# Optimization experiments

Hardware: AMD Instinct MI355X
Metric: run time of the kernel (lower is better)

The kernel has to match this reference:

```python
import jax, jax.numpy as jnp
import numpy as np

N, E, D, K = 60000, 1200000, 64, 3

def setup_inputs() -> dict:
    key = jax.random.key(0)
    k1, k2, k3 = jax.random.split(key, 3)
    feat = jax.random.normal(k1, (N, D), dtype=jnp.float32)
    src = jax.random.randint(k2, (E,), 0, N)
    dst = jax.random.randint(k3, (E,), 0, N)
    lambda_max = jnp.ones((1,), dtype=jnp.float32)
    return {"feat": feat, "src": src, "dst": dst, "lambda_max": lambda_max}

def reference(feat, src, dst, lambda_max):
    n = feat.shape[0]
    # in-degree of each node = number of edges whose dst is that node
    deg = jax.ops.segment_sum(jnp.ones(src.shape[0], dtype=feat.dtype), dst, num_segments=n)
    d_invsqrt = jnp.maximum(deg, 1.0) ** -0.5  # [N]
    d_invsqrt = d_invsqrt[:, None]             # [N,1]
    re_norm = 2.0 / lambda_max                 # [1], broadcasts over nodes/feats

    def unn_laplacian(x):
        # x * D^-1/2 A D^-1/2 via gather over src, scatter-sum to dst
        return d_invsqrt * jax.ops.segment_sum((x * d_invsqrt)[src], dst, num_segments=n)

    X0 = feat
    outs = [X0]
    if K > 1:
        h = unn_laplacian(X0)
        X1 = -re_norm * h + X0 * (re_norm - 1.0)
        outs.append(X1)
    for _ in range(2, K):
        h = unn_laplacian(X1)
        Xi = -2.0 * re_norm * h + X1 * 2.0 * (re_norm - 1.0) - X0
        outs.append(Xi)
        X1, X0 = Xi, X1
    Xt = jnp.concatenate(outs, axis=1)  # [N, K*D]
    return jax.nn.relu(Xt)
```

## Files before the change

kernel.cpp:

```cpp
#include <hip/hip_runtime.h>


#define DF 64
#define BCAP 5760
#define EPT 32

__device__ __forceinline__ unsigned bf16rne(float f) {
    unsigned u = __float_as_uint(f);
    return (u + 0x7FFFu + ((u >> 16) & 1u)) >> 16;
}
__device__ __forceinline__ float bflo(unsigned u) { return __uint_as_float(u << 16); }
__device__ __forceinline__ float bfhi(unsigned u) { return __uint_as_float(u & 0xFFFF0000u); }

__global__ __launch_bounds__(256) void partition_kernel(
    const int* __restrict__ src, const int* __restrict__ dst,
    int* __restrict__ bcursor, int* __restrict__ staged, int E) {
    __shared__ int hist[256];
    __shared__ int base[256];
    int tid = threadIdx.x;
    hist[tid] = 0;
    __syncthreads();
    int e0 = blockIdx.x * (256 * EPT);
    int val[EPT]; int rb[EPT]; int rr[EPT];
    #pragma unroll
    for (int k = 0; k < EPT / 4; k++) {
        int e = e0 + (k * 256 + tid) * 4;
        if (e + 3 < E) {
            int4 s4 = *(const int4*)(src + e);
            int4 d4 = *(const int4*)(dst + e);
            int ss[4] = {s4.x, s4.y, s4.z, s4.w};
            int dd[4] = {d4.x, d4.y, d4.z, d4.w};
            #pragma unroll
            for (int j = 0; j < 4; j++) {
                int b = dd[j] >> 8;
                val[k * 4 + j] = (ss[j] << 8) | (dd[j] & 255);
                rb[k * 4 + j] = b;
                rr[k * 4 + j] = atomicAdd(&hist[b], 1);
            }
        } else {
            #pragma unroll
            for (int j = 0; j < 4; j++) {
                int e1 = e + j;
                if (e1 < E) {
                    int s = src[e1], d = dst[e1];
                    int b = d >> 8;
                    val[k * 4 + j] = (s << 8) | (d & 255);
                    rb[k * 4 + j] = b;
                    rr[k * 4 + j] = atomicAdd(&hist[b], 1);
                } else rb[k * 4 + j] = -1;
            }
        }
    }
    __syncthreads();
    int h = hist[tid];
    base[tid] = h ? atomicAdd(&bcursor[tid], h) : 0;
    __syncthreads();
    #pragma unroll
    for (int k = 0; k < EPT; k++) {
        if (rb[k] >= 0) {
            int pos = base[rb[k]] + rr[k];
            if (pos < BCAP) staged[rb[k] * BCAP + pos] = val[k];
        }
    }
}

__global__ __launch_bounds__(256) void bucket_csr_kernel(
    const int* __restrict__ staged, const int* __restrict__ bcursor,
    int* __restrict__ col, int2* __restrict__ begend,
    float* __restrict__ dinv, int n) {
    __shared__ int sin[BCAP];
    __shared__ __align__(16) int sout[BCAP];
    __shared__ int hist[256];
    __shared__ int scn[256];
    __shared__ int cur[256];
    int tid = threadIdx.x;
    int b = blockIdx.x;
    int cnt = bcursor[b]; if (cnt > BCAP) cnt = BCAP;
    hist[tid] = 0;
    __syncthreads();
    const int* sb = staged + b * BCAP;
    for (int i = tid; i < cnt; i += 256) {
        int e = sb[i];
        sin[i] = e;
        atomicAdd(&hist[e & 255], 1);
    }
    __syncthreads();
    int v = hist[tid];
    scn[tid] = v;
    __syncthreads();
    for (int off = 1; off < 256; off <<= 1) {
        int x = scn[tid];
        int y = (tid >= off) ? scn[tid - off] : 0;
        __syncthreads();
        scn[tid] = x + y;
        __syncthreads();
    }
    int excl = scn[tid] - v;
    cur[tid] = excl;
    __syncthreads();
    for (int i = tid; i < cnt; i += 256) {
        int e = sin[i];
        int pos = atomicAdd(&cur[e & 255], 1);
        sout[pos] = e >> 8;
    }
    __syncthreads();
    int* cb = col + b * BCAP;
    int cnt4 = cnt >> 2;
    for (int i = tid; i < cnt4; i += 256)
        *(int4*)(cb + i * 4) = *(const int4*)(sout + i * 4);
    for (int i = (cnt4 << 2) + tid; i < cnt; i += 256) cb[i] = sout[i];
    int node = (b << 8) + tid;
    if (node < n) {
        int d = hist[tid];
        begend[node] = make_int2(b * BCAP + excl, b * BCAP + excl + d);
        if (d < 1) d = 1;
        dinv[node] = rsqrtf((float)d);
    }
}

__global__ __launch_bounds__(256) void convert_kernel(
    const float* __restrict__ feat, uint2* __restrict__ featb, int total8) {
    int i = blockIdx.x * 256 + threadIdx.x;
    if (i >= total8) return;
    float4 a = *(const float4*)(feat + (size_t)i * 8);
    float4 b = *(const float4*)(feat + (size_t)i * 8 + 4);
    uint2 o;
    (void)o;
    uint4 p;
    p.x = bf16rne(a.x) | (bf16rne(a.y) << 16);
    p.y = bf16rne(a.z) | (bf16rne(a.w) << 16);
    p.z = bf16rne(b.x) | (bf16rne(b.y) << 16);
    p.w = bf16rne(b.z) | (bf16rne(b.w) << 16);
    *(uint4*)((unsigned*)featb + (size_t)i * 4) = p;
}

__global__ __launch_bounds__(256) void prop1_kernel(
    const float* __restrict__ feat, const uint2* __restrict__ featb,
    const int2* __restrict__ begend, const int* __restrict__ col,
    const float* __restrict__ dinv, const float* __restrict__ lambda_max,
    uint2* __restrict__ x1n, float* __restrict__ out, int n) {
    int node = (int)((blockIdx.x * blockDim.x + threadIdx.x) >> 6);
    if (node >= n) return;
    int lane = threadIdx.x & 63;
    int grp = lane >> 4;
    int sub = lane & 15;
    int2 be = begend[node];
    int beg = be.x, end = be.y;
    float4 x0 = *(const float4*)(feat + (size_t)node * DF + sub * 4);
    float dn = dinv[node];
    float rn = 2.0f / lambda_max[0];
    float ax = 0.f, ay = 0.f, az = 0.f, aw = 0.f;
    int i = beg + grp;
    for (; i + 12 < end; i += 16) {
        int s0 = col[i], s1 = col[i + 4], s2 = col[i + 8], s3 = col[i + 12];
        uint2 v0 = featb[(size_t)s0 * 16 + sub];
        uint2 v1 = featb[(size_t)s1 * 16 + sub];
        uint2 v2 = featb[(size_t)s2 * 16 + sub];
        uint2 v3 = featb[(size_t)s3 * 16 + sub];
        float w0 = dinv[s0], w1 = dinv[s1], w2 = dinv[s2], w3 = dinv[s3];
        ax += bflo(v0.x) * w0 + bflo(v1.x) * w1 + bflo(v2.x) * w2 + bflo(v3.x) * w3;
        ay += bfhi(v0.x) * w0 + bfhi(v1.x) * w1 + bfhi(v2.x) * w2 + bfhi(v3.x) * w3;
        az += bflo(v0.y) * w0 + bflo(v1.y) * w1 + bflo(v2.y) * w2 + bflo(v3.y) * w3;
        aw += bfhi(v0.y) * w0 + bfhi(v1.y) * w1 + bfhi(v2.y) * w2 + bfhi(v3.y) * w3;
    }
    for (; i < end; i += 4) {
        int s0 = col[i];
        uint2 v0 = featb[(size_t)s0 * 16 + sub];
        float w0 = dinv[s0];
        ax += bflo(v0.x) * w0; ay += bfhi(v0.x) * w0;
        az += bflo(v0.y) * w0; aw += bfhi(v0.y) * w0;
    }
    ax += __shfl_xor(ax, 16); ax += __shfl_xor(ax, 32);
    ay += __shfl_xor(ay, 16); ay += __shfl_xor(ay, 32);
    az += __shfl_xor(az, 16); az += __shfl_xor(az, 32);
    aw += __shfl_xor(aw, 16); aw += __shfl_xor(aw, 32);
    if (grp == 0) {
        float c1 = rn - 1.0f;
        float4 x1v;
        x1v.x = c1 * x0.x - rn * dn * ax;
        x1v.y = c1 * x0.y - rn * dn * ay;
        x1v.z = c1 * x0.z - rn * dn * az;
        x1v.w = c1 * x0.w - rn * dn * aw;
        uint2 p;
        p.x = bf16rne(x1v.x) | (bf16rne(x1v.y) << 16);
        p.y = bf16rne(x1v.z) | (bf16rne(x1v.w) << 16);
        x1n[(size_t)node * 16 + sub] = p;
        size_t o = (size_t)node * (3 * DF);
        float4 r0 = make_float4(fmaxf(x0.x, 0.f), fmaxf(x0.y, 0.f), fmaxf(x0.z, 0.f), fmaxf(x0.w, 0.f));
        float4 r1 = make_float4(fmaxf(x1v.x, 0.f), fmaxf(x1v.y, 0.f), fmaxf(x1v.z, 0.f), fmaxf(x1v.w, 0.f));
        *(float4*)(out + o + sub * 4) = r0;
        *(float4*)(out + o + DF + sub * 4) = r1;
    }
}

__global__ __launch_bounds__(256) void prop2_kernel(
    const float* __restrict__ feat, const uint2* __restrict__ x1n,
    const int2* __restrict__ begend, const int* __restrict__ col,
    const float* __restrict__ dinv, const float* __restrict__ lambda_max,
    float* __restrict__ out, int n) {
    int node = (int)((blockIdx.x * blockDim.x + threadIdx.x) >> 6);
    if (node >= n) return;
    int lane = threadIdx.x & 63;
    int grp = lane >> 4;
    int sub = lane & 15;
    int2 be = begend[node];
    int beg = be.x, end = be.y;
    float4 x0 = *(const float4*)(feat + (size_t)node * DF + sub * 4);
    uint2 xo = x1n[(size_t)node * 16 + sub];
    float dn = dinv[node];
    float rn = 2.0f / lambda_max[0];
    float ax = 0.f, ay = 0.f, az = 0.f, aw = 0.f;
    int i = beg + grp;
    for (; i + 12 < end; i += 16) {
        int s0 = col[i], s1 = col[i + 4], s2 = col[i + 8], s3 = col[i + 12];
        uint2 v0 = x1n[(size_t)s0 * 16 + sub];
        uint2 v1 = x1n[(size_t)s1 * 16 + sub];
        uint2 v2 = x1n[(size_t)s2 * 16 + sub];
        uint2 v3 = x1n[(size_t)s3 * 16 + sub];
        float w0 = dinv[s0], w1 = dinv[s1], w2 = dinv[s2], w3 = dinv[s3];
        ax += bflo(v0.x) * w0 + bflo(v1.x) * w1 + bflo(v2.x) * w2 + bflo(v3.x) * w3;
        ay += bfhi(v0.x) * w0 + bfhi(v1.x) * w1 + bfhi(v2.x) * w2 + bfhi(v3.x) * w3;
        az += bflo(v0.y) * w0 + bflo(v1.y) * w1 + bflo(v2.y) * w2 + bflo(v3.y) * w3;
        aw += bfhi(v0.y) * w0 + bfhi(v1.y) * w1 + bfhi(v2.y) * w2 + bfhi(v3.y) * w3;
    }
    for (; i < end; i += 4) {
        int s0 = col[i];
        uint2 v0 = x1n[(size_t)s0 * 16 + sub];
        float w0 = dinv[s0];
        ax += bflo(v0.x) * w0; ay += bfhi(v0.x) * w0;
        az += bflo(v0.y) * w0; aw += bfhi(v0.y) * w0;
    }
    ax += __shfl_xor(ax, 16); ax += __shfl_xor(ax, 32);
    ay += __shfl_xor(ay, 16); ay += __shfl_xor(ay, 32);
    az += __shfl_xor(az, 16); az += __shfl_xor(az, 32);
    aw += __shfl_xor(aw, 16); aw += __shfl_xor(aw, 32);
    if (grp == 0) {
        float c2 = 2.0f * (rn - 1.0f);
        float4 x1v = make_float4(bflo(xo.x), bfhi(xo.x), bflo(xo.y), bfhi(xo.y));
        float4 x2v;
        x2v.x = c2 * x1v.x - 2.0f * rn * dn * ax - x0.x;
        x2v.y = c2 * x1v.y - 2.0f * rn * dn * ay - x0.y;
        x2v.z = c2 * x1v.z - 2.0f * rn * dn * az - x0.z;
        x2v.w = c2 * x1v.w - 2.0f * rn * dn * aw - x0.w;
        size_t o = (size_t)node * (3 * DF);
        float4 r2 = make_float4(fmaxf(x2v.x, 0.f), fmaxf(x2v.y, 0.f), fmaxf(x2v.z, 0.f), fmaxf(x2v.w, 0.f));
        *(float4*)(out + o + 2 * DF + sub * 4) = r2;
    }
}

extern "C" void kernel_launch(void* const* d_in, const int* in_sizes, int n_in,
                              void* d_out, int out_size, void* d_ws, size_t ws_size,
                              hipStream_t stream) {
    const float* feat = (const float*)d_in[0];
    const int* src = (const int*)d_in[1];
    const int* dst = (const int*)d_in[2];
    const float* lambda_max = (const float*)d_in[3];
    const int n = in_sizes[0] / DF;
    const int E = in_sizes[1];
    float* out = (float*)d_out;

    const int nb = (n + 255) >> 8;

    auto align256 = [](size_t x) { return (x + 255) & ~(size_t)255; };
    char* ws = (char*)d_ws;
    int* bcursor = (int*)ws;  ws += align256(256 * sizeof(int));
    float* dinv = (float*)ws; ws += align256((size_t)n * sizeof(float));
    int2* begend = (int2*)ws; ws += align256((size_t)n * sizeof(int2));
    int* col = (int*)ws;      ws += align256((size_t)nb * BCAP * sizeof(int));
    int* staged = (int*)ws;
    uint2* featb = (uint2*)ws; ws += align256((size_t)n * DF * 2);
    uint2* x1n = (uint2*)ws;

    hipMemsetAsync(bcursor, 0, 256 * sizeof(int), stream);
    partition_kernel<<<(E + 256 * EPT - 1) / (256 * EPT), 256, 0, stream>>>(
        src, dst, bcursor, staged, E);
    bucket_csr_kernel<<<nb, 256, 0, stream>>>(staged, bcursor, col, begend, dinv, n);
    convert_kernel<<<(n * DF / 8 + 255) / 256, 256, 0, stream>>>(feat, featb, n * DF / 8);
    prop1_kernel<<<(n + 3) / 4, 256, 0, stream>>>(feat, featb, begend, col, dinv, lambda_max, x1n, out, n);
    prop2_kernel<<<(n + 3) / 4, 256, 0, stream>>>(feat, x1n, begend, col, dinv, lambda_max, out, n);
}
```

Measured before the change: 174.7 us.

## Fuse all graph-build and propagation stages into one cooperative persistent kernel

Replaces the memset and five separate launches (partition, bucket CSR, bf16 convert, two propagation passes) with a single cooperative kernel. The stages are separated by grid-wide syncs, and the grid is sized from occupancy across 256 CUs. Shared memory for the partition and CSR phases is overlaid in a union, and the partition tile is halved (EPT 16). The staged buffer now gets its own workspace region because the conversion runs first. The aim is to remove launch gaps and inter-kernel drain. The cost is lower occupancy: the roughly 48KB shared-memory union applies to the gather phases too, which then run as grid-stride loops with grid.sync overhead.

```diff
diff --git a/kernel.cpp b/kernel.cpp
--- a/kernel.cpp
+++ b/kernel.cpp
@@ -1,9 +1,12 @@
 #include <hip/hip_runtime.h>
+#include <hip/hip_cooperative_groups.h>
+
+namespace cg = cooperative_groups;
 
 
 #define DF 64
 #define BCAP 5760
-#define EPT 32
+#define EPT 16
 
 __device__ __forceinline__ unsigned bf16rne(float f) {
     unsigned u = __float_as_uint(f);
@@ -12,239 +15,235 @@
 __device__ __forceinline__ float bflo(unsigned u) { return __uint_as_float(u << 16); }
 __device__ __forceinline__ float bfhi(unsigned u) { return __uint_as_float(u & 0xFFFF0000u); }
 
-__global__ __launch_bounds__(256) void partition_kernel(
-    const int* __restrict__ src, const int* __restrict__ dst,
-    int* __restrict__ bcursor, int* __restrict__ staged, int E) {
-    __shared__ int hist[256];
-    __shared__ int base[256];
-    int tid = threadIdx.x;
-    hist[tid] = 0;
-    __syncthreads();
-    int e0 = blockIdx.x * (256 * EPT);
-    int val[EPT]; int rb[EPT]; int rr[EPT];
-    #pragma unroll
-    for (int k = 0; k < EPT / 4; k++) {
-        int e = e0 + (k * 256 + tid) * 4;
-        if (e + 3 < E) {
-            int4 s4 = *(const int4*)(src + e);
-            int4 d4 = *(const int4*)(dst + e);
-            int ss[4] = {s4.x, s4.y, s4.z, s4.w};
-            int dd[4] = {d4.x, d4.y, d4.z, d4.w};
-            #pragma unroll
-            for (int j = 0; j < 4; j++) {
-                int b = dd[j] >> 8;
-                val[k * 4 + j] = (ss[j] << 8) | (dd[j] & 255);
-                rb[k * 4 + j] = b;
-                rr[k * 4 + j] = atomicAdd(&hist[b], 1);
+__global__ __launch_bounds__(256) void fused_kernel(
+    const float* __restrict__ feat, const int* __restrict__ src,
+    const int* __restrict__ dst, const float* __restrict__ lambda_max,
+    int* __restrict__ bcursor, int* __restrict__ staged,
+    int* __restrict__ col, int2* __restrict__ begend,
+    float* __restrict__ dinv, uint2* __restrict__ featb,
+    uint2* __restrict__ x1n, float* __restrict__ out,
+    int n, int E, int nb, int nRounds) {
+    __shared__ __align__(16) union {
+        struct { int hist[256]; int base[256]; } part;
+        struct { int sin[BCAP]; int sout[BCAP]; int hist[256]; int scn[256]; int cur[256]; } csr;
+    } sh;
+    cg::grid_group grid = cg::this_grid();
+    const int tid = threadIdx.x;
+    const int gsize = gridDim.x;
+
+    if (blockIdx.x == 0) bcursor[tid] = 0;
+    {
+        int total8 = n * DF / 8;
+        for (int i = blockIdx.x * 256 + tid; i < total8; i += gsize * 256) {
+            float4 a = *(const float4*)(feat + (size_t)i * 8);
+            float4 b = *(const float4*)(feat + (size_t)i * 8 + 4);
+            uint4 p;
+            p.x = bf16rne(a.x) | (bf16rne(a.y) << 16);
+            p.y = bf16rne(a.z) | (bf16rne(a.w) << 16);
+            p.z = bf16rne(b.x) | (bf16rne(b.y) << 16);
+            p.w = bf16rne(b.z) | (bf16rne(b.w) << 16);
+            *(uint4*)((unsigned*)featb + (size_t)i * 4) = p;
+        }
+    }
+    grid.sync();
+
+    for (int r = blockIdx.x; r < nRounds; r += gsize) {
+        sh.part.hist[tid] = 0;
+        __syncthreads();
+        int e0 = r * (256 * EPT);
+        int val[EPT]; int rb[EPT]; int rr[EPT];
+        #pragma unroll
+        for (int k = 0; k < EPT / 4; k++) {
+            int e = e0 + (k * 256 + tid) * 4;
+            if (e + 3 < E) {
+                int4 s4 = *(const int4*)(src + e);
+                int4 d4 = *(const int4*)(dst + e);
+                int ss[4] = {s4.x, s4.y, s4.z, s4.w};
+                int dd[4] = {d4.x, d4.y, d4.z, d4.w};
+                #pragma unroll
+                for (int j = 0; j < 4; j++) {
+                    int b = dd[j] >> 8;
+                    val[k * 4 + j] = (ss[j] << 8) | (dd[j] & 255);
+                    rb[k * 4 + j] = b;
+                    rr[k * 4 + j] = atomicAdd(&sh.part.hist[b], 1);
+                }
+            } else {
+                #pragma unroll
+                for (int j = 0; j < 4; j++) {
+                    int e1 = e + j;
+                    if (e1 < E) {
+                        int s = src[e1], d = dst[e1];
+                        int b = d >> 8;
+                        val[k * 4 + j] = (s << 8) | (d & 255);
+                        rb[k * 4 + j] = b;
+                        rr[k * 4 + j] = atomicAdd(&sh.part.hist[b], 1);
+                    } else rb[k * 4 + j] = -1;
+                }
             }
-        } else {
-            #pragma unroll
-            for (int j = 0; j < 4; j++) {
-                int e1 = e + j;
-                if (e1 < E) {
-                    int s = src[e1], d = dst[e1];
-                    int b = d >> 8;
-                    val[k * 4 + j] = (s << 8) | (d & 255);
-                    rb[k * 4 + j] = b;
-                    rr[k * 4 + j] = atomicAdd(&hist[b], 1);
-                } else rb[k * 4 + j] = -1;
+        }
+        __syncthreads();
+        int h = sh.part.hist[tid];
+        sh.part.base[tid] = h ? atomicAdd(&bcursor[tid], h) : 0;
+        __syncthreads();
+        #pragma unroll
+        for (int k = 0; k < EPT; k++) {
+            if (rb[k] >= 0) {
+                int pos = sh.part.base[rb[k]] + rr[k];
+                if (pos < BCAP) staged[rb[k] * BCAP + pos] = val[k];
             }
         }
-    }
-    __syncthreads();
-    int h = hist[tid];
-    base[tid] = h ? atomicAdd(&bcursor[tid], h) : 0;
-    __syncthreads();
-    #pragma unroll
-    for (int k = 0; k < EPT; k++) {
-        if (rb[k] >= 0) {
-            int pos = base[rb[k]] + rr[k];
-            if (pos < BCAP) staged[rb[k] * BCAP + pos] = val[k];
-        }
-    }
-}
-
-__global__ __launch_bounds__(256) void bucket_csr_kernel(
-    const int* __restrict__ staged, const int* __restrict__ bcursor,
-    int* __restrict__ col, int2* __restrict__ begend,
-    float* __restrict__ dinv, int n) {
-    __shared__ int sin[BCAP];
-    __shared__ __align__(16) int sout[BCAP];
-    __shared__ int hist[256];
-    __shared__ int scn[256];
-    __shared__ int cur[256];
-    int tid = threadIdx.x;
-    int b = blockIdx.x;
-    int cnt = bcursor[b]; if (cnt > BCAP) cnt = BCAP;
-    hist[tid] = 0;
-    __syncthreads();
-    const int* sb = staged + b * BCAP;
-    for (int i = tid; i < cnt; i += 256) {
-        int e = sb[i];
-        sin[i] = e;
-        atomicAdd(&hist[e & 255], 1);
-    }
-    __syncthreads();
-    int v = hist[tid];
-    scn[tid] = v;
-    __syncthreads();
-    for (int off = 1; off < 256; off <<= 1) {
-        int x = scn[tid];
-        int y = (tid >= off) ? scn[tid - off] : 0;
-        __syncthreads();
-        scn[tid] = x + y;
-        __syncthreads();
-    }
-    int excl = scn[tid] - v;
-    cur[tid] = excl;
-    __syncthreads();
-    for (int i = tid; i < cnt; i += 256) {
-        int e = sin[i];
-        int pos = atomicAdd(&cur[e & 255], 1);
-        sout[pos] = e >> 8;
-    }
-    __syncthreads();
-    int* cb = col + b * BCAP;
-    int cnt4 = cnt >> 2;
-    for (int i = tid; i < cnt4; i += 256)
-        *(int4*)(cb + i * 4) = *(const int4*)(sout + i * 4);
-    for (int i = (cnt4 << 2) + tid; i < cnt; i += 256) cb[i] = sout[i];
-    int node = (b << 8) + tid;
-    if (node < n) {
-        int d = hist[tid];
-        begend[node] = make_int2(b * BCAP + excl, b * BCAP + excl + d);
-        if (d < 1) d = 1;
-        dinv[node] = rsqrtf((float)d);
-    }
-}
-
-__global__ __launch_bounds__(256) void convert_kernel(
-    const float* __restrict__ feat, uint2* __restrict__ featb, int total8) {
-    int i = blockIdx.x * 256 + threadIdx.x;
-    if (i >= total8) return;
-    float4 a = *(const float4*)(feat + (size_t)i * 8);
-    float4 b = *(const float4*)(feat + (size_t)i * 8 + 4);
-    uint2 o;
-    (void)o;
-    uint4 p;
-    p.x = bf16rne(a.x) | (bf16rne(a.y) << 16);
-    p.y = bf16rne(a.z) | (bf16rne(a.w) << 16);
-    p.z = bf16rne(b.x) | (bf16rne(b.y) << 16);
-    p.w = bf16rne(b.z) | (bf16rne(b.w) << 16);
-    *(uint4*)((unsigned*)featb + (size_t)i * 4) = p;
-}
-
-__global__ __launch_bounds__(256) void prop1_kernel(
-    const float* __restrict__ feat, const uint2* __restrict__ featb,
-    const int2* __restrict__ begend, const int* __restrict__ col,
-    const float* __restrict__ dinv, const float* __restrict__ lambda_max,
-    uint2* __restrict__ x1n, float* __restrict__ out, int n) {
-    int node = (int)((blockIdx.x * blockDim.x + threadIdx.x) >> 6);
-    if (node >= n) return;
-    int lane = threadIdx.x & 63;
-    int grp = lane >> 4;
-    int sub = lane & 15;
-    int2 be = begend[node];
-    int beg = be.x, end = be.y;
-    float4 x0 = *(const float4*)(feat + (size_t)node * DF + sub * 4);
-    float dn = dinv[node];
-    float rn = 2.0f / lambda_max[0];
-    float ax = 0.f, ay = 0.f, az = 0.f, aw = 0.f;
-    int i = beg + grp;
-    for (; i + 12 < end; i += 16) {
-        int s0 = col[i], s1 = col[i + 4], s2 = col[i + 8], s3 = col[i + 12];
-        uint2 v0 = featb[(size_t)s0 * 16 + sub];
-        uint2 v1 = featb[(size_t)s1 * 16 + sub];
-        uint2 v2 = featb[(size_t)s2 * 16 + sub];
-        uint2 v3 = featb[(size_t)s3 * 16 + sub];
-        float w0 = dinv[s0], w1 = dinv[s1], w2 = dinv[s2], w3 = dinv[s3];
-        ax += bflo(v0.x) * w0 + bflo(v1.x) * w1 + bflo(v2.x) * w2 + bflo(v3.x) * w3;
-        ay += bfhi(v0.x) * w0 + bfhi(v1.x) * w1 + bfhi(v2.x) * w2 + bfhi(v3.x) * w3;
-        az += bflo(v0.y) * w0 + bflo(v1.y) * w1 + bflo(v2.y) * w2 + bflo(v3.y) * w3;
-        aw += bfhi(v0.y) * w0 + bfhi(v1.y) * w1 + bfhi(v2.y) * w2 + bfhi(v3.y) * w3;
-    }
-    for (; i < end; i += 4) {
-        int s0 = col[i];
-        uint2 v0 = featb[(size_t)s0 * 16 + sub];
-        float w0 = dinv[s0];
-        ax += bflo(v0.x) * w0; ay += bfhi(v0.x) * w0;
-        az += bflo(v0.y) * w0; aw += bfhi(v0.y) * w0;
-    }
-    ax += __shfl_xor(ax, 16); ax += __shfl_xor(ax, 32);
-    ay += __shfl_xor(ay, 16); ay += __shfl_xor(ay, 32);
-    az += __shfl_xor(az, 16); az += __shfl_xor(az, 32);
-    aw += __shfl_xor(aw, 16); aw += __shfl_xor(aw, 32);
-    if (grp == 0) {
-        float c1 = rn - 1.0f;
-        float4 x1v;
-        x1v.x = c1 * x0.x - rn * dn * ax;
-        x1v.y = c1 * x0.y - rn * dn * ay;
-        x1v.z = c1 * x0.z - rn * dn * az;
-        x1v.w = c1 * x0.w - rn * dn * aw;
-        uint2 p;
-        p.x = bf16rne(x1v.x) | (bf16rne(x1v.y) << 16);
-        p.y = bf16rne(x1v.z) | (bf16rne(x1v.w) << 16);
-        x1n[(size_t)node * 16 + sub] = p;
-        size_t o = (size_t)node * (3 * DF);
-        float4 r0 = make_float4(fmaxf(x0.x, 0.f), fmaxf(x0.y, 0.f), fmaxf(x0.z, 0.f), fmaxf(x0.w, 0.f));
-        float4 r1 = make_float4(fmaxf(x1v.x, 0.f), fmaxf(x1v.y, 0.f), fmaxf(x1v.z, 0.f), fmaxf(x1v.w, 0.f));
-        *(float4*)(out + o + sub * 4) = r0;
-        *(float4*)(out + o + DF + sub * 4) = r1;
-    }
-}
-
-__global__ __launch_bounds__(256) void prop2_kernel(
-    const float* __restrict__ feat, const uint2* __restrict__ x1n,
-    const int2* __restrict__ begend, const int* __restrict__ col,
-    const float* __restrict__ dinv, const float* __restrict__ lambda_max,
-    float* __restrict__ out, int n) {
-    int node = (int)((blockIdx.x * blockDim.x + threadIdx.x) >> 6);
-    if (node >= n) return;
-    int lane = threadIdx.x & 63;
-    int grp = lane >> 4;
-    int sub = lane & 15;
-    int2 be = begend[node];
-    int beg = be.x, end = be.y;
-    float4 x0 = *(const float4*)(feat + (size_t)node * DF + sub * 4);
-    uint2 xo = x1n[(size_t)node * 16 + sub];
-    float dn = dinv[node];
-    float rn = 2.0f / lambda_max[0];
-    float ax = 0.f, ay = 0.f, az = 0.f, aw = 0.f;
-    int i = beg + grp;
-    for (; i + 12 < end; i += 16) {
-        int s0 = col[i], s1 = col[i + 4], s2 = col[i + 8], s3 = col[i + 12];
-        uint2 v0 = x1n[(size_t)s0 * 16 + sub];
-        uint2 v1 = x1n[(size_t)s1 * 16 + sub];
-        uint2 v2 = x1n[(size_t)s2 * 16 + sub];
-        uint2 v3 = x1n[(size_t)s3 * 16 + sub];
-        float w0 = dinv[s0], w1 = dinv[s1], w2 = dinv[s2], w3 = dinv[s3];
-        ax += bflo(v0.x) * w0 + bflo(v1.x) * w1 + bflo(v2.x) * w2 + bflo(v3.x) * w3;
-        ay += bfhi(v0.x) * w0 + bfhi(v1.x) * w1 + bfhi(v2.x) * w2 + bfhi(v3.x) * w3;
-        az += bflo(v0.y) * w0 + bflo(v1.y) * w1 + bflo(v2.y) * w2 + bflo(v3.y) * w3;
-        aw += bfhi(v0.y) * w0 + bfhi(v1.y) * w1 + bfhi(v2.y) * w2 + bfhi(v3.y) * w3;
-    }
-    for (; i < end; i += 4) {
-        int s0 = col[i];
-        uint2 v0 = x1n[(size_t)s0 * 16 + sub];
-        float w0 = dinv[s0];
-        ax += bflo(v0.x) * w0; ay += bfhi(v0.x) * w0;
-        az += bflo(v0.y) * w0; aw += bfhi(v0.y) * w0;
-    }
-    ax += __shfl_xor(ax, 16); ax += __shfl_xor(ax, 32);
-    ay += __shfl_xor(ay, 16); ay += __shfl_xor(ay, 32);
-    az += __shfl_xor(az, 16); az += __shfl_xor(az, 32);
-    aw += __shfl_xor(aw, 16); aw += __shfl_xor(aw, 32);
-    if (grp == 0) {
-        float c2 = 2.0f * (rn - 1.0f);
-        float4 x1v = make_float4(bflo(xo.x), bfhi(xo.x), bflo(xo.y), bfhi(xo.y));
-        float4 x2v;
-        x2v.x = c2 * x1v.x - 2.0f * rn * dn * ax - x0.x;
-        x2v.y = c2 * x1v.y - 2.0f * rn * dn * ay - x0.y;
-        x2v.z = c2 * x1v.z - 2.0f * rn * dn * az - x0.z;
-        x2v.w = c2 * x1v.w - 2.0f * rn * dn * aw - x0.w;
-        size_t o = (size_t)node * (3 * DF);
-        float4 r2 = make_float4(fmaxf(x2v.x, 0.f), fmaxf(x2v.y, 0.f), fmaxf(x2v.z, 0.f), fmaxf(x2v.w, 0.f));
-        *(float4*)(out + o + 2 * DF + sub * 4) = r2;
+        __syncthreads();
+    }
+    grid.sync();
+
+    for (int b = blockIdx.x; b < nb; b += gsize) {
+        int cnt = bcursor[b]; if (cnt > BCAP) cnt = BCAP;
+        sh.csr.hist[tid] = 0;
+        __syncthreads();
+        const int* sb = staged + b * BCAP;
+        for (int i = tid; i < cnt; i += 256) {
+            int e = sb[i];
+            sh.csr.sin[i] = e;
+            atomicAdd(&sh.csr.hist[e & 255], 1);
+        }
+        __syncthreads();
+        int v = sh.csr.hist[tid];
+        sh.csr.scn[tid] = v;
+        __syncthreads();
+        for (int off = 1; off < 256; off <<= 1) {
+            int x = sh.csr.scn[tid];
+            int y = (tid >= off) ? sh.csr.scn[tid - off] : 0;
+            __syncthreads();
+            sh.csr.scn[tid] = x + y;
+            __syncthreads();
+        }
+        int excl = sh.csr.scn[tid] - v;
+        sh.csr.cur[tid] = excl;
+        __syncthreads();
+        for (int i = tid; i < cnt; i += 256) {
+            int e = sh.csr.sin[i];
+            int pos = atomicAdd(&sh.csr.cur[e & 255], 1);
+            sh.csr.sout[pos] = e >> 8;
+        }
+        __syncthreads();
+        int* cb = col + b * BCAP;
+        int cnt4 = cnt >> 2;
+        for (int i = tid; i < cnt4; i += 256)
+            *(int4*)(cb + i * 4) = *(const int4*)(sh.csr.sout + i * 4);
+        for (int i = (cnt4 << 2) + tid; i < cnt; i += 256) cb[i] = sh.csr.sout[i];
+        int node = (b << 8) + tid;
+        if (node < n) {
+            int d = sh.csr.hist[tid];
+            begend[node] = make_int2(b * BCAP + excl, b * BCAP + excl + d);
+            if (d < 1) d = 1;
+            dinv[node] = rsqrtf((float)d);
+        }
+        __syncthreads();
+    }
+    grid.sync();
+
+    const int lane = tid & 63;
+    const int grp = lane >> 4;
+    const int sub = lane & 15;
+    const int wid = (blockIdx.x * 256 + tid) >> 6;
+    const int nW = (gsize * 256) >> 6;
+    const float rn = 2.0f / lambda_max[0];
+
+    for (int node = wid; node < n; node += nW) {
+        int2 be = begend[node];
+        int beg = be.x, end = be.y;
+        float4 x0 = *(const float4*)(feat + (size_t)node * DF + sub * 4);
+        float dn = dinv[node];
+        float ax = 0.f, ay = 0.f, az = 0.f, aw = 0.f;
+        int i = beg + grp;
+        for (; i + 12 < end; i += 16) {
+            int s0 = col[i], s1 = col[i + 4], s2 = col[i + 8], s3 = col[i + 12];
+            uint2 v0 = featb[(size_t)s0 * 16 + sub];
+            uint2 v1 = featb[(size_t)s1 * 16 + sub];
+            uint2 v2 = featb[(size_t)s2 * 16 + sub];
+            uint2 v3 = featb[(size_t)s3 * 16 + sub];
+            float w0 = dinv[s0], w1 = dinv[s1], w2 = dinv[s2], w3 = dinv[s3];
+            ax += bflo(v0.x) * w0 + bflo(v1.x) * w1 + bflo(v2.x) * w2 + bflo(v3.x) * w3;
+            ay += bfhi(v0.x) * w0 + bfhi(v1.x) * w1 + bfhi(v2.x) * w2 + bfhi(v3.x) * w3;
+            az += bflo(v0.y) * w0 + bflo(v1.y) * w1 + bflo(v2.y) * w2 + bflo(v3.y) * w3;
+            aw += bfhi(v0.y) * w0 + bfhi(v1.y) * w1 + bfhi(v2.y) * w2 + bfhi(v3.y) * w3;
+        }
+        for (; i < end; i += 4) {
+            int s0 = col[i];
+            uint2 v0 = featb[(size_t)s0 * 16 + sub];
+            float w0 = dinv[s0];
+            ax += bflo(v0.x) * w0; ay += bfhi(v0.x) * w0;
+            az += bflo(v0.y) * w0; aw += bfhi(v0.y) * w0;
+        }
+        ax += __shfl_xor(ax, 16); ax += __shfl_xor(ax, 32);
+        ay += __shfl_xor(ay, 16); ay += __shfl_xor(ay, 32);
+        az += __shfl_xor(az, 16); az += __shfl_xor(az, 32);
+        aw += __shfl_xor(aw, 16); aw += __shfl_xor(aw, 32);
+        if (grp == 0) {
+            float c1 = rn - 1.0f;
+            float dnrn = rn * dn;
+            float4 x1v;
+            x1v.x = c1 * x0.x - dnrn * ax;
+            x1v.y = c1 * x0.y - dnrn * ay;
+            x1v.z = c1 * x0.z - dnrn * az;
+            x1v.w = c1 * x0.w - dnrn * aw;
+            uint2 p;
+            p.x = bf16rne(x1v.x) | (bf16rne(x1v.y) << 16);
+            p.y = bf16rne(x1v.z) | (bf16rne(x1v.w) << 16);
+            x1n[(size_t)node * 16 + sub] = p;
+            size_t o = (size_t)node * (3 * DF);
+            float4 r0 = make_float4(fmaxf(x0.x, 0.f), fmaxf(x0.y, 0.f), fmaxf(x0.z, 0.f), fmaxf(x0.w, 0.f));
+            float4 r1 = make_float4(fmaxf(x1v.x, 0.f), fmaxf(x1v.y, 0.f), fmaxf(x1v.z, 0.f), fmaxf(x1v.w, 0.f));
+            *(float4*)(out + o + sub * 4) = r0;
+            *(float4*)(out + o + DF + sub * 4) = r1;
+        }
+    }
+    grid.sync();
+
+    for (int node = wid; node < n; node += nW) {
+        int2 be = begend[node];
+        int beg = be.x, end = be.y;
+        float4 x0 = *(const float4*)(feat + (size_t)node * DF + sub * 4);
+        uint2 xo = x1n[(size_t)node * 16 + sub];
+        float dn = dinv[node];
+        float ax = 0.f, ay = 0.f, az = 0.f, aw = 0.f;
+        int i = beg + grp;
+        for (; i + 12 < end; i += 16) {
+            int s0 = col[i], s1 = col[i + 4], s2 = col[i + 8], s3 = col[i + 12];
+            uint2 v0 = x1n[(size_t)s0 * 16 + sub];
+            uint2 v1 = x1n[(size_t)s1 * 16 + sub];
+            uint2 v2 = x1n[(size_t)s2 * 16 + sub];
+            uint2 v3 = x1n[(size_t)s3 * 16 + sub];
+            float w0 = dinv[s0], w1 = dinv[s1], w2 = dinv[s2], w3 = dinv[s3];
+            ax += bflo(v0.x) * w0 + bflo(v1.x) * w1 + bflo(v2.x) * w2 + bflo(v3.x) * w3;
+            ay += bfhi(v0.x) * w0 + bfhi(v1.x) * w1 + bfhi(v2.x) * w2 + bfhi(v3.x) * w3;
+            az += bflo(v0.y) * w0 + bflo(v1.y) * w1 + bflo(v2.y) * w2 + bflo(v3.y) * w3;
+            aw += bfhi(v0.y) * w0 + bfhi(v1.y) * w1 + bfhi(v2.y) * w2 + bfhi(v3.y) * w3;
+        }
+        for (; i < end; i += 4) {
+            int s0 = col[i];
+            uint2 v0 = x1n[(size_t)s0 * 16 + sub];
+            float w0 = dinv[s0];
+            ax += bflo(v0.x) * w0; ay += bfhi(v0.x) * w0;
+            az += bflo(v0.y) * w0; aw += bfhi(v0.y) * w0;
+        }
+        ax += __shfl_xor(ax, 16); ax += __shfl_xor(ax, 32);
+        ay += __shfl_xor(ay, 16); ay += __shfl_xor(ay, 32);
+        az += __shfl_xor(az, 16); az += __shfl_xor(az, 32);
+        aw += __shfl_xor(aw, 16); aw += __shfl_xor(aw, 32);
+        if (grp == 0) {
+            float c2 = 2.0f * (rn - 1.0f);
+            float s2c = 2.0f * rn * dn;
+            float4 x1v = make_float4(bflo(xo.x), bfhi(xo.x), bflo(xo.y), bfhi(xo.y));
+            float4 x2v;
+            x2v.x = c2 * x1v.x - s2c * ax - x0.x;
+            x2v.y = c2 * x1v.y - s2c * ay - x0.y;
+            x2v.z = c2 * x1v.z - s2c * az - x0.z;
+            x2v.w = c2 * x1v.w - s2c * aw - x0.w;
+            size_t o = (size_t)node * (3 * DF);
+            float4 r2 = make_float4(fmaxf(x2v.x, 0.f), fmaxf(x2v.y, 0.f), fmaxf(x2v.z, 0.f), fmaxf(x2v.w, 0.f));
+            *(float4*)(out + o + 2 * DF + sub * 4) = r2;
+        }
     }
 }
 
@@ -255,27 +254,33 @@
     const int* src = (const int*)d_in[1];
     const int* dst = (const int*)d_in[2];
     const float* lambda_max = (const float*)d_in[3];
-    const int n = in_sizes[0] / DF;
-    const int E = in_sizes[1];
+    int n = in_sizes[0] / DF;
+    int E = in_sizes[1];
     float* out = (float*)d_out;
 
-    const int nb = (n + 255) >> 8;
+    int nb = (n + 255) >> 8;
+    int nRounds = (E + 256 * EPT - 1) / (256 * EPT);
 
     auto align256 = [](size_t x) { return (x + 255) & ~(size_t)255; };
     char* ws = (char*)d_ws;
-    int* bcursor = (int*)ws;  ws += align256(256 * sizeof(int));
-    float* dinv = (float*)ws; ws += align256((size_t)n * sizeof(float));
-    int2* begend = (int2*)ws; ws += align256((size_t)n * sizeof(int2));
-    int* col = (int*)ws;      ws += align256((size_t)nb * BCAP * sizeof(int));
-    int* staged = (int*)ws;
+    int* bcursor = (int*)ws;   ws += align256(256 * sizeof(int));
+    float* dinv = (float*)ws;  ws += align256((size_t)n * sizeof(float));
+    int2* begend = (int2*)ws;  ws += align256((size_t)n * sizeof(int2));
+    int* col = (int*)ws;       ws += align256((size_t)nb * BCAP * sizeof(int));
+    int* staged = (int*)ws;    ws += align256((size_t)nb * BCAP * sizeof(int));
     uint2* featb = (uint2*)ws; ws += align256((size_t)n * DF * 2);
     uint2* x1n = (uint2*)ws;
 
-    hipMemsetAsync(bcursor, 0, 256 * sizeof(int), stream);
-    partition_kernel<<<(E + 256 * EPT - 1) / (256 * EPT), 256, 0, stream>>>(
-        src, dst, bcursor, staged, E);
-    bucket_csr_kernel<<<nb, 256, 0, stream>>>(staged, bcursor, col, begend, dinv, n);
-    convert_kernel<<<(n * DF / 8 + 255) / 256, 256, 0, stream>>>(feat, featb, n * DF / 8);
-    prop1_kernel<<<(n + 3) / 4, 256, 0, stream>>>(feat, featb, begend, col, dinv, lambda_max, x1n, out, n);
-    prop2_kernel<<<(n + 3) / 4, 256, 0, stream>>>(feat, x1n, begend, col, dinv, lambda_max, out, n);
+    int bpc = 0;
+    if (hipOccupancyMaxActiveBlocksPerMultiprocessor(&bpc, fused_kernel, 256, 0)
+            != hipSuccess || bpc < 1)
+        bpc = 1;
+    int gridBlocks = bpc * 256;
+
+    void* args[] = {(void*)&feat, (void*)&src, (void*)&dst, (void*)&lambda_max,
+                    (void*)&bcursor, (void*)&staged, (void*)&col, (void*)&begend,
+                    (void*)&dinv, (void*)&featb, (void*)&x1n, (void*)&out,
+                    (void*)&n, (void*)&E, (void*)&nb, (void*)&nRounds};
+    hipLaunchCooperativeKernel((void*)fused_kernel, dim3(gridBlocks), dim3(256),
+                               args, 0, stream);
 }
```

Result: slower. 490.9 us (+181.0%).

## Pre-scale gathered features by dinv and fuse bf16 conversion into CSR build

Applied to the files above, without the earlier changes.

Source features are now pre-multiplied by D^-1/2 when they are converted to bf16, and that conversion moves into the bucket CSR kernel, so one launch goes away. X1 is stored pre-scaled by dinv so both propagation passes gather with no per-edge dinv[src] loads or multiplies. This cuts a random 4-byte load per edge in each pass, at the cost of extra bf16 rounding of scaled values and a divide by dn to recover X1 in prop2. The staged buffer no longer aliases featb, which the fused conversion requires, so workspace use grows.

```diff
diff --git a/kernel.cpp b/kernel.cpp
--- a/kernel.cpp
+++ b/kernel.cpp
@@ -66,13 +66,15 @@
 
 __global__ __launch_bounds__(256) void bucket_csr_kernel(
     const int* __restrict__ staged, const int* __restrict__ bcursor,
+    const float* __restrict__ feat,
     int* __restrict__ col, int2* __restrict__ begend,
-    float* __restrict__ dinv, int n) {
+    float* __restrict__ dinv, uint2* __restrict__ featb, int n) {
     __shared__ int sin[BCAP];
     __shared__ __align__(16) int sout[BCAP];
     __shared__ int hist[256];
     __shared__ int scn[256];
     __shared__ int cur[256];
+    __shared__ float sdinv[256];
     int tid = threadIdx.x;
     int b = blockIdx.x;
     int cnt = bcursor[b]; if (cnt > BCAP) cnt = BCAP;
@@ -110,28 +112,32 @@
         *(int4*)(cb + i * 4) = *(const int4*)(sout + i * 4);
     for (int i = (cnt4 << 2) + tid; i < cnt; i += 256) cb[i] = sout[i];
     int node = (b << 8) + tid;
+    float dv = 1.0f;
     if (node < n) {
         int d = hist[tid];
         begend[node] = make_int2(b * BCAP + excl, b * BCAP + excl + d);
         if (d < 1) d = 1;
-        dinv[node] = rsqrtf((float)d);
-    }
-}
-
-__global__ __launch_bounds__(256) void convert_kernel(
-    const float* __restrict__ feat, uint2* __restrict__ featb, int total8) {
-    int i = blockIdx.x * 256 + threadIdx.x;
-    if (i >= total8) return;
-    float4 a = *(const float4*)(feat + (size_t)i * 8);
-    float4 b = *(const float4*)(feat + (size_t)i * 8 + 4);
-    uint2 o;
-    (void)o;
-    uint4 p;
-    p.x = bf16rne(a.x) | (bf16rne(a.y) << 16);
-    p.y = bf16rne(a.z) | (bf16rne(a.w) << 16);
-    p.z = bf16rne(b.x) | (bf16rne(b.y) << 16);
-    p.w = bf16rne(b.z) | (bf16rne(b.w) << 16);
-    *(uint4*)((unsigned*)featb + (size_t)i * 4) = p;
+        dv = rsqrtf((float)d);
+        dinv[node] = dv;
+    }
+    sdinv[tid] = dv;
+    __syncthreads();
+    int base_node = b << 8;
+    int rows = n - base_node; if (rows > 256) rows = 256;
+    int subl = tid & 15;
+    #pragma unroll 4
+    for (int p = 0; p < 16; p++) {
+        int nl = p * 16 + (tid >> 4);
+        if (nl < rows) {
+            float w = sdinv[nl];
+            const float* fr = feat + (size_t)(base_node + nl) * DF + subl * 4;
+            float4 a = *(const float4*)fr;
+            uint2 pk;
+            pk.x = bf16rne(a.x * w) | (bf16rne(a.y * w) << 16);
+            pk.y = bf16rne(a.z * w) | (bf16rne(a.w * w) << 16);
+            featb[(size_t)(base_node + nl) * 16 + subl] = pk;
+        }
+    }
 }
 
 __global__ __launch_bounds__(256) void prop1_kernel(
@@ -157,18 +163,16 @@
         uint2 v1 = featb[(size_t)s1 * 16 + sub];
         uint2 v2 = featb[(size_t)s2 * 16 + sub];
         uint2 v3 = featb[(size_t)s3 * 16 + sub];
-        float w0 = dinv[s0], w1 = dinv[s1], w2 = dinv[s2], w3 = dinv[s3];
-        ax += bflo(v0.x) * w0 + bflo(v1.x) * w1 + bflo(v2.x) * w2 + bflo(v3.x) * w3;
-        ay += bfhi(v0.x) * w0 + bfhi(v1.x) * w1 + bfhi(v2.x) * w2 + bfhi(v3.x) * w3;
-        az += bflo(v0.y) * w0 + bflo(v1.y) * w1 + bflo(v2.y) * w2 + bflo(v3.y) * w3;
-        aw += bfhi(v0.y) * w0 + bfhi(v1.y) * w1 + bfhi(v2.y) * w2 + bfhi(v3.y) * w3;
+        ax += bflo(v0.x) + bflo(v1.x) + bflo(v2.x) + bflo(v3.x);
+        ay += bfhi(v0.x) + bfhi(v1.x) + bfhi(v2.x) + bfhi(v3.x);
+        az += bflo(v0.y) + bflo(v1.y) + bflo(v2.y) + bflo(v3.y);
+        aw += bfhi(v0.y) + bfhi(v1.y) + bfhi(v2.y) + bfhi(v3.y);
     }
     for (; i < end; i += 4) {
         int s0 = col[i];
         uint2 v0 = featb[(size_t)s0 * 16 + sub];
-        float w0 = dinv[s0];
-        ax += bflo(v0.x) * w0; ay += bfhi(v0.x) * w0;
-        az += bflo(v0.y) * w0; aw += bfhi(v0.y) * w0;
+        ax += bflo(v0.x); ay += bfhi(v0.x);
+        az += bflo(v0.y); aw += bfhi(v0.y);
     }
     ax += __shfl_xor(ax, 16); ax += __shfl_xor(ax, 32);
     ay += __shfl_xor(ay, 16); ay += __shfl_xor(ay, 32);
@@ -176,14 +180,15 @@
     aw += __shfl_xor(aw, 16); aw += __shfl_xor(aw, 32);
     if (grp == 0) {
         float c1 = rn - 1.0f;
+        float dnrn = rn * dn;
         float4 x1v;
-        x1v.x = c1 * x0.x - rn * dn * ax;
-        x1v.y = c1 * x0.y - rn * dn * ay;
-        x1v.z = c1 * x0.z - rn * dn * az;
-        x1v.w = c1 * x0.w - rn * dn * aw;
+        x1v.x = c1 * x0.x - dnrn * ax;
+        x1v.y = c1 * x0.y - dnrn * ay;
+        x1v.z = c1 * x0.z - dnrn * az;
+        x1v.w = c1 * x0.w - dnrn * aw;
         uint2 p;
-        p.x = bf16rne(x1v.x) | (bf16rne(x1v.y) << 16);
-        p.y = bf16rne(x1v.z) | (bf16rne(x1v.w) << 16);
+        p.x = bf16rne(x1v.x * dn) | (bf16rne(x1v.y * dn) << 16);
+        p.y = bf16rne(x1v.z * dn) | (bf16rne(x1v.w * dn) << 16);
         x1n[(size_t)node * 16 + sub] = p;
         size_t o = (size_t)node * (3 * DF);
         float4 r0 = make_float4(fmaxf(x0.x, 0.f), fmaxf(x0.y, 0.f), fmaxf(x0.z, 0.f), fmaxf(x0.w, 0.f));
@@ -217,18 +222,16 @@
         uint2 v1 = x1n[(size_t)s1 * 16 + sub];
         uint2 v2 = x1n[(size_t)s2 * 16 + sub];
         uint2 v3 = x1n[(size_t)s3 * 16 + sub];
-        float w0 = dinv[s0], w1 = dinv[s1], w2 = dinv[s2], w3 = dinv[s3];
-        ax += bflo(v0.x) * w0 + bflo(v1.x) * w1 + bflo(v2.x) * w2 + bflo(v3.x) * w3;
-        ay += bfhi(v0.x) * w0 + bfhi(v1.x) * w1 + bfhi(v2.x) * w2 + bfhi(v3.x) * w3;
-        az += bflo(v0.y) * w0 + bflo(v1.y) * w1 + bflo(v2.y) * w2 + bflo(v3.y) * w3;
-        aw += bfhi(v0.y) * w0 + bfhi(v1.y) * w1 + bfhi(v2.y) * w2 + bfhi(v3.y) * w3;
+        ax += bflo(v0.x) + bflo(v1.x) + bflo(v2.x) + bflo(v3.x);
+        ay += bfhi(v0.x) + bfhi(v1.x) + bfhi(v2.x) + bfhi(v3.x);
+        az += bflo(v0.y) + bflo(v1.y) + bflo(v2.y) + bflo(v3.y);
+        aw += bfhi(v0.y) + bfhi(v1.y) + bfhi(v2.y) + bfhi(v3.y);
     }
     for (; i < end; i += 4) {
         int s0 = col[i];
         uint2 v0 = x1n[(size_t)s0 * 16 + sub];
-        float w0 = dinv[s0];
-        ax += bflo(v0.x) * w0; ay += bfhi(v0.x) * w0;
-        az += bflo(v0.y) * w0; aw += bfhi(v0.y) * w0;
+        ax += bflo(v0.x); ay += bfhi(v0.x);
+        az += bflo(v0.y); aw += bfhi(v0.y);
     }
     ax += __shfl_xor(ax, 16); ax += __shfl_xor(ax, 32);
     ay += __shfl_xor(ay, 16); ay += __shfl_xor(ay, 32);
@@ -236,12 +239,15 @@
     aw += __shfl_xor(aw, 16); aw += __shfl_xor(aw, 32);
     if (grp == 0) {
         float c2 = 2.0f * (rn - 1.0f);
-        float4 x1v = make_float4(bflo(xo.x), bfhi(xo.x), bflo(xo.y), bfhi(xo.y));
+        float s2c = 2.0f * rn * dn;
+        float inv_dn = 1.0f / dn;
+        float4 x1v = make_float4(bflo(xo.x) * inv_dn, bfhi(xo.x) * inv_dn,
+                                 bflo(xo.y) * inv_dn, bfhi(xo.y) * inv_dn);
         float4 x2v;
-        x2v.x = c2 * x1v.x - 2.0f * rn * dn * ax - x0.x;
-        x2v.y = c2 * x1v.y - 2.0f * rn * dn * ay - x0.y;
-        x2v.z = c2 * x1v.z - 2.0f * rn * dn * az - x0.z;
-        x2v.w = c2 * x1v.w - 2.0f * rn * dn * aw - x0.w;
+        x2v.x = c2 * x1v.x - s2c * ax - x0.x;
+        x2v.y = c2 * x1v.y - s2c * ay - x0.y;
+        x2v.z = c2 * x1v.z - s2c * az - x0.z;
+        x2v.w = c2 * x1v.w - s2c * aw - x0.w;
         size_t o = (size_t)node * (3 * DF);
         float4 r2 = make_float4(fmaxf(x2v.x, 0.f), fmaxf(x2v.y, 0.f), fmaxf(x2v.z, 0.f), fmaxf(x2v.w, 0.f));
         *(float4*)(out + o + 2 * DF + sub * 4) = r2;
@@ -263,19 +269,21 @@
 
     auto align256 = [](size_t x) { return (x + 255) & ~(size_t)255; };
     char* ws = (char*)d_ws;
-    int* bcursor = (int*)ws;  ws += align256(256 * sizeof(int));
-    float* dinv = (float*)ws; ws += align256((size_t)n * sizeof(float));
-    int2* begend = (int2*)ws; ws += align256((size_t)n * sizeof(int2));
-    int* col = (int*)ws;      ws += align256((size_t)nb * BCAP * sizeof(int));
-    int* staged = (int*)ws;
+    int* bcursor = (int*)ws;   ws += align256(256 * sizeof(int));
+    float* dinv = (float*)ws;  ws += align256((size_t)n * sizeof(float));
+    int2* begend = (int2*)ws;  ws += align256((size_t)n * sizeof(int2));
+    int* col = (int*)ws;       ws += align256((size_t)nb * BCAP * sizeof(int));
+    int* staged = (int*)ws;    ws += align256((size_t)nb * BCAP * sizeof(int));
     uint2* featb = (uint2*)ws; ws += align256((size_t)n * DF * 2);
     uint2* x1n = (uint2*)ws;
 
     hipMemsetAsync(bcursor, 0, 256 * sizeof(int), stream);
     partition_kernel<<<(E + 256 * EPT - 1) / (256 * EPT), 256, 0, stream>>>(
         src, dst, bcursor, staged, E);
-    bucket_csr_kernel<<<nb, 256, 0, stream>>>(staged, bcursor, col, begend, dinv, n);
-    convert_kernel<<<(n * DF / 8 + 255) / 256, 256, 0, stream>>>(feat, featb, n * DF / 8);
-    prop1_kernel<<<(n + 3) / 4, 256, 0, stream>>>(feat, featb, begend, col, dinv, lambda_max, x1n, out, n);
-    prop2_kernel<<<(n + 3) / 4, 256, 0, stream>>>(feat, x1n, begend, col, dinv, lambda_max, out, n);
-}
+    bucket_csr_kernel<<<nb, 256, 0, stream>>>(staged, bcursor, feat, col,
+                                              begend, dinv, featb, n);
+    prop1_kernel<<<(n + 3) / 4, 256, 0, stream>>>(feat, featb, begend, col,
+                                                  dinv, lambda_max, x1n, out, n);
+    prop2_kernel<<<(n + 3) / 4, 256, 0, stream>>>(feat, x1n, begend, col,
+                                                  dinv, lambda_max, out, n);
+}
```

Measured after the change: 178.2 us. Within noise of the previous version (+2.0%).
